# Kernel tuning notes

Measured on AMD Instinct MI355X. Metric: run time of the kernel, lower is better.

The kernel has to match this reference:

```python
import jax, jax.numpy as jnp
import numpy as np
from jax import lax

NUM_CLASSES = 5  # config['training']['num_classes_per_task']
EMBED_DIM = 64


def _conv(x, w, b, pad):
    y = lax.conv_general_dilated(x, w, (1, 1), [(pad, pad), (pad, pad)],
                                 dimension_numbers=('NCHW', 'OIHW', 'NCHW'))
    return y + b[None, :, None, None]


def _maxpool2(x):
    n, c, h, w = x.shape
    return x.reshape(n, c, h // 2, 2, w // 2, 2).max(axis=(3, 5))


def _lenet(x, c1w, c1b, c2w, c2b, f1w, f1b, f2w, f2b, f3w, f3b):
    h = _maxpool2(jax.nn.relu(_conv(x, c1w, c1b, pad=2)))   # [N,6,14,14]
    h = _maxpool2(jax.nn.relu(_conv(h, c2w, c2b, pad=0)))   # [N,16,5,5]
    h = h.reshape(h.shape[0], -1)                            # [N,400]
    h = jax.nn.relu(h @ f1w.T + f1b)                         # [N,120]
    h = jax.nn.relu(h @ f2w.T + f2b)                         # [N,84]
    return h @ f3w.T + f3b                                   # [N,64]


def setup_inputs() -> dict:
    key = jax.random.key(0)
    ks = jax.random.split(key, 12)
    s = 0.1
    return {
        'x': jax.random.normal(ks[0], (20480, 1, 28, 28), dtype=jnp.float32),
        'c1w': jax.random.normal(ks[1], (6, 1, 5, 5), dtype=jnp.float32) * s,
        'c1b': jnp.zeros((6,), dtype=jnp.float32),
        'c2w': jax.random.normal(ks[2], (16, 6, 5, 5), dtype=jnp.float32) * s,
        'c2b': jnp.zeros((16,), dtype=jnp.float32),
        'f1w': jax.random.normal(ks[3], (120, 400), dtype=jnp.float32) * s,
        'f1b': jnp.zeros((120,), dtype=jnp.float32),
        'f2w': jax.random.normal(ks[4], (84, 120), dtype=jnp.float32) * s,
        'f2b': jnp.zeros((84,), dtype=jnp.float32),
        'f3w': jax.random.normal(ks[5], (EMBED_DIM, 84), dtype=jnp.float32) * s,
        'f3b': jnp.zeros((EMBED_DIM,), dtype=jnp.float32),
    }


def reference(x, c1w, c1b, c2w, c2b, f1w, f1b, f2w, f2b, f3w, f3b):
    emb = _lenet(x, c1w, c1b, c2w, c2b, f1w, f1b, f2w, f2b, f3w, f3b)  # [N,D]
    # Source builds a flat prototypes list of all N*D scalars / num_classes,
    # but only indices 0..D-1 are ever read -> first embedding row / num_classes.
    proto = emb[0] / NUM_CLASSES                     # [D]
    s = jax.nn.softmax(emb, axis=1)                  # softmax over dim 1
    # fun_L(x, p) = sqrt((x-p)^2) = |x-p|
    logits = jnp.abs(s - proto[None, :])             # [N,D]
    batch_size = x.shape[0] // NUM_CLASSES
    return logits.reshape(batch_size, NUM_CLASSES, -1)
```

## Files before the change

kernel.cpp:

```cpp
#include <hip/hip_runtime.h>


__device__ __forceinline__ int xcd_swizzle(int orig, int nwg) {
    int xcd = orig & 7, q = nwg >> 3, r = nwg & 7;
    int base = (xcd < r) ? xcd * (q + 1) : r * (q + 1) + (xcd - r) * q;
    return base + (orig >> 3);
}

__global__ __launch_bounds__(256) void transpose_x(
    const float* __restrict__ x, float* __restrict__ xt, int nc)
{
    __shared__ float t[64][65];
    const int tx = threadIdx.x & 63, ty = threadIdx.x >> 6;
    const int p0 = blockIdx.x * 64, n0 = blockIdx.y * 64;
    #pragma unroll
    for (int rr = 0; rr < 16; ++rr) {
        int nl = rr * 4 + ty;
        int pp = p0 + tx;
        int pr = pp >> 5, pc = pp & 31;
        float v = 0.f;
        if (pr >= 2 && pr < 30 && pc >= 2 && pc < 30)
            v = x[(size_t)(n0 + nl) * 784 + (pr - 2) * 28 + (pc - 2)];
        t[tx][nl] = v;
    }
    __syncthreads();
    #pragma unroll
    for (int rr = 0; rr < 16; ++rr) {
        int pl = rr * 4 + ty;
        xt[(size_t)(p0 + pl) * nc + n0 + tx] = t[pl][tx];
    }
}

__global__ __launch_bounds__(256, 2) void conv1_bt(
    const float* __restrict__ xt, const float* __restrict__ c1w,
    const float* __restrict__ c1b, float* __restrict__ p1t, int nc)
{
    const int newid = xcd_swizzle(blockIdx.x, gridDim.x);
    const int grp = newid / 196, pos = newid - grp * 196;
    const int py = pos / 14, px = pos - py * 14;
    const int img = grp * 512 + threadIdx.x * 2;
    const float* pb = xt + (size_t)((2 * py) * 32 + 2 * px) * nc + img;

    float2 acc[24];
    #pragma unroll
    for (int i = 0; i < 24; ++i) acc[i] = make_float2(0.f, 0.f);

    #pragma unroll
    for (int r = 0; r < 6; ++r) {
        float2 row[6];
        #pragma unroll
        for (int cc = 0; cc < 6; ++cc)
            row[cc] = *(const float2*)&pb[(size_t)(r * 32 + cc) * nc];
        #pragma unroll
        for (int ch = 0; ch < 6; ++ch) {
            const float* wp = c1w + ch * 25;
            if (r <= 4) {
                #pragma unroll
                for (int kx = 0; kx < 5; ++kx) {
                    float w = wp[r * 5 + kx];
                    acc[ch*4+0].x += row[kx].x   * w;
                    acc[ch*4+0].y += row[kx].y   * w;
                    acc[ch*4+1].x += row[kx+1].x * w;
                    acc[ch*4+1].y += row[kx+1].y * w;
                }
            }
            if (r >= 1) {
                #pragma unroll
                for (int kx = 0; kx < 5; ++kx) {
                    float w = wp[(r - 1) * 5 + kx];
                    acc[ch*4+2].x += row[kx].x   * w;
                    acc[ch*4+2].y += row[kx].y   * w;
                    acc[ch*4+3].x += row[kx+1].x * w;
                    acc[ch*4+3].y += row[kx+1].y * w;
                }
            }
        }
    }
    #pragma unroll
    for (int ch = 0; ch < 6; ++ch) {
        float b = c1b[ch];
        float mx = fmaxf(fmaxf(acc[ch*4+0].x, acc[ch*4+1].x),
                         fmaxf(acc[ch*4+2].x, acc[ch*4+3].x)) + b;
        float my = fmaxf(fmaxf(acc[ch*4+0].y, acc[ch*4+1].y),
                         fmaxf(acc[ch*4+2].y, acc[ch*4+3].y)) + b;
        float2 o2 = make_float2(fmaxf(mx, 0.f), fmaxf(my, 0.f));
        *(float2*)&p1t[(size_t)(ch * 196 + pos) * nc + img] = o2;
    }
}

__global__ __launch_bounds__(256, 2) void conv2_bt(
    const float* __restrict__ p1t, const float* __restrict__ c2w,
    const float* __restrict__ c2b, float* __restrict__ ht, int nc)
{
    const int newid = xcd_swizzle(blockIdx.x, gridDim.x);
    const int grp = newid / 25, pos = newid - grp * 25;
    const int qy = pos / 5, qx = pos - qy * 5;
    const int img = grp * 256 + threadIdx.x;
    const int y0 = 2 * qy, x0 = 2 * qx;

    float acc[64];
    #pragma unroll
    for (int i = 0; i < 64; ++i) acc[i] = 0.f;

    #pragma unroll 1
    for (int ci = 0; ci < 6; ++ci) {
        const float* pb = p1t + (size_t)(ci * 196 + y0 * 14 + x0) * nc + img;
        #pragma unroll
        for (int r = 0; r < 6; ++r) {
            float row[6];
            #pragma unroll
            for (int cc = 0; cc < 6; ++cc)
                row[cc] = pb[(size_t)(r * 14 + cc) * nc];
            #pragma unroll
            for (int oc = 0; oc < 16; ++oc) {
                const float* wp = c2w + (oc * 6 + ci) * 25;
                if (r <= 4) {
                    #pragma unroll
                    for (int kx = 0; kx < 5; ++kx) {
                        float w = wp[r * 5 + kx];
                        acc[oc*4+0] += row[kx]   * w;
                        acc[oc*4+1] += row[kx+1] * w;
                    }
                }
                if (r >= 1) {
                    #pragma unroll
                    for (int kx = 0; kx < 5; ++kx) {
                        float w = wp[(r - 1) * 5 + kx];
                        acc[oc*4+2] += row[kx]   * w;
                        acc[oc*4+3] += row[kx+1] * w;
                    }
                }
            }
        }
    }
    #pragma unroll
    for (int oc = 0; oc < 16; ++oc) {
        float b = c2b[oc];
        float m = fmaxf(fmaxf(acc[oc*4+0], acc[oc*4+1]),
                        fmaxf(acc[oc*4+2], acc[oc*4+3])) + b;
        ht[(size_t)(oc * 25 + pos) * nc + img] = fmaxf(m, 0.f);
    }
}

__global__ __launch_bounds__(256) void fc1_bt(
    const float* __restrict__ ht, const float* __restrict__ f1w,
    const float* __restrict__ f1b, float* __restrict__ a1t, int nc)
{
    const int newid = xcd_swizzle(blockIdx.x, gridDim.x);
    const int grp = newid / 15, og = newid - grp * 15;
    const int img = grp * 512 + threadIdx.x * 2;
    const float* wb = f1w + og * 8 * 400;

    float2 acc[8];
    #pragma unroll
    for (int j = 0; j < 8; ++j) acc[j] = make_float2(0.f, 0.f);

    #pragma unroll 4
    for (int k = 0; k < 400; ++k) {
        float2 hv = *(const float2*)&ht[(size_t)k * nc + img];
        #pragma unroll
        for (int j = 0; j < 8; ++j) {
            float w = wb[j * 400 + k];
            acc[j].x += hv.x * w;
            acc[j].y += hv.y * w;
        }
    }
    #pragma unroll
    for (int j = 0; j < 8; ++j) {
        int o = og * 8 + j;
        float b = f1b[o];
        float2 o2 = make_float2(fmaxf(acc[j].x + b, 0.f),
                                fmaxf(acc[j].y + b, 0.f));
        *(float2*)&a1t[(size_t)o * nc + img] = o2;
    }
}

__global__ __launch_bounds__(256) void fc2_bt(
    const float* __restrict__ a1t, const float* __restrict__ f2w,
    const float* __restrict__ f2b, float* __restrict__ a2t, int nc)
{
    const int newid = xcd_swizzle(blockIdx.x, gridDim.x);
    const int grp = newid / 12, og = newid - grp * 12;
    const int img = grp * 512 + threadIdx.x * 2;
    const float* wb = f2w + og * 7 * 120;

    float2 acc[7];
    #pragma unroll
    for (int j = 0; j < 7; ++j) acc[j] = make_float2(0.f, 0.f);

    #pragma unroll 4
    for (int k = 0; k < 120; ++k) {
        float2 hv = *(const float2*)&a1t[(size_t)k * nc + img];
        #pragma unroll
        for (int j = 0; j < 7; ++j) {
            float w = wb[j * 120 + k];
            acc[j].x += hv.x * w;
            acc[j].y += hv.y * w;
        }
    }
    #pragma unroll
    for (int j = 0; j < 7; ++j) {
        int o = og * 7 + j;
        float b = f2b[o];
        float2 o2 = make_float2(fmaxf(acc[j].x + b, 0.f),
                                fmaxf(acc[j].y + b, 0.f));
        *(float2*)&a2t[(size_t)o * nc + img] = o2;
    }
}

__global__ __launch_bounds__(256) void fc3_bt(
    const float* __restrict__ a2t, const float* __restrict__ f3w,
    const float* __restrict__ f3b, float* __restrict__ embt,
    int nc, int Ntot, int n0)
{
    const int newid = xcd_swizzle(blockIdx.x, gridDim.x);
    const int grp = newid / 8, og = newid - grp * 8;
    const int limg = grp * 512 + threadIdx.x * 2;
    const float* wb = f3w + og * 8 * 84;

    float2 acc[8];
    #pragma unroll
    for (int j = 0; j < 8; ++j) acc[j] = make_float2(0.f, 0.f);

    #pragma unroll 4
    for (int k = 0; k < 84; ++k) {
        float2 hv = *(const float2*)&a2t[(size_t)k * nc + limg];
        #pragma unroll
        for (int j = 0; j < 8; ++j) {
            float w = wb[j * 84 + k];
            acc[j].x += hv.x * w;
            acc[j].y += hv.y * w;
        }
    }
    #pragma unroll
    for (int j = 0; j < 8; ++j) {
        int o = og * 8 + j;
        float b = f3b[o];
        float2 o2 = make_float2(acc[j].x + b, acc[j].y + b);
        *(float2*)&embt[(size_t)o * Ntot + n0 + limg] = o2;
    }
}

__global__ __launch_bounds__(256) void proto_head_t(
    const float* __restrict__ embt, float* __restrict__ out, int N)
{
    const int img = blockIdx.x * 256 + threadIdx.x;
    float v[64];
    float m = -1e30f;
    #pragma unroll
    for (int o = 0; o < 64; ++o) {
        v[o] = embt[(size_t)o * N + img];
        m = fmaxf(m, v[o]);
    }
    float s = 0.f;
    #pragma unroll
    for (int o = 0; o < 64; ++o) {
        v[o] = __expf(v[o] - m);
        s += v[o];
    }
    float inv = __frcp_rn(s);
    #pragma unroll
    for (int o = 0; o < 64; o += 4) {
        float4 r;
        r.x = fabsf(v[o+0] * inv - embt[(size_t)(o+0) * N] * 0.2f);
        r.y = fabsf(v[o+1] * inv - embt[(size_t)(o+1) * N] * 0.2f);
        r.z = fabsf(v[o+2] * inv - embt[(size_t)(o+2) * N] * 0.2f);
        r.w = fabsf(v[o+3] * inv - embt[(size_t)(o+3) * N] * 0.2f);
        *(float4*)&out[(size_t)img * 64 + o] = r;
    }
}

extern "C" void kernel_launch(void* const* d_in, const int* in_sizes, int n_in,
                              void* d_out, int out_size, void* d_ws, size_t ws_size,
                              hipStream_t stream)
{
    const float* x   = (const float*)d_in[0];
    const float* c1w = (const float*)d_in[1];
    const float* c1b = (const float*)d_in[2];
    const float* c2w = (const float*)d_in[3];
    const float* c2b = (const float*)d_in[4];
    const float* f1w = (const float*)d_in[5];
    const float* f1b = (const float*)d_in[6];
    const float* f2w = (const float*)d_in[7];
    const float* f2b = (const float*)d_in[8];
    const float* f3w = (const float*)d_in[9];
    const float* f3b = (const float*)d_in[10];
    float* out = (float*)d_out;

    const int N = in_sizes[0] / 784;
    float* base = (float*)d_ws;

    int c = 40;
    const int cands[] = {1, 2, 4, 5, 8, 10, 20, 40};
    for (int k = 0; k < 8; ++k) {
        int cd = cands[k];
        if (N % cd) continue;
        int ncq = N / cd;
        if (ncq % 512) continue;
        size_t need = (size_t)8800 * ncq + (size_t)256 * N;
        if (need <= ws_size) { c = cd; break; }
    }
    const int nc = N / c;

    float* xt   = base;
    float* p1t  = base + (size_t)1024 * nc;
    float* ht_  = base;
    float* a1t  = p1t;
    float* a2t  = p1t + (size_t)120 * nc;
    float* embt = base + (size_t)2200 * nc;

    for (int k = 0; k < c; ++k) {
        int n0 = k * nc;
        transpose_x<<<dim3(16, nc / 64), 256, 0, stream>>>(
            x + (size_t)n0 * 784, xt, nc);
        conv1_bt<<<196 * (nc / 512), 256, 0, stream>>>(
            xt, c1w, c1b, p1t, nc);
        conv2_bt<<<25 * (nc / 256), 256, 0, stream>>>(
            p1t, c2w, c2b, ht_, nc);
        fc1_bt<<<15 * (nc / 512), 256, 0, stream>>>(
            ht_, f1w, f1b, a1t, nc);
        fc2_bt<<<12 * (nc / 512), 256, 0, stream>>>(
            a1t, f2w, f2b, a2t, nc);
        fc3_bt<<<8 * (nc / 512), 256, 0, stream>>>(
            a2t, f3w, f3b, embt, nc, N, n0);
    }
    proto_head_t<<<N / 256, 256, 0, stream>>>(embt, out, N);
}
```

Baseline: 296.0 us.

## Split conv1 and conv2 output channels across blocks, process two images per thread

conv1 now splits its 6 output channels into two passes of 3 handled by separate blocks, halving the accumulator registers per thread. conv2 splits its 16 output channels into four groups of 4 and switches to float2 loads so each thread handles two images. The aim is lower register pressure, more blocks in flight, and wider memory accesses in conv2. The cost is that input rows are reloaded once per channel group (2x for conv1, 4x for conv2), which adds global or cache traffic.

```diff
diff --git a/kernel.cpp b/kernel.cpp
--- a/kernel.cpp
+++ b/kernel.cpp
@@ -36,14 +36,15 @@
     const float* __restrict__ c1b, float* __restrict__ p1t, int nc)
 {
     const int newid = xcd_swizzle(blockIdx.x, gridDim.x);
-    const int grp = newid / 196, pos = newid - grp * 196;
+    const int grp = newid / 392, rem = newid - grp * 392;
+    const int pass = rem / 196, pos = rem - pass * 196;
     const int py = pos / 14, px = pos - py * 14;
     const int img = grp * 512 + threadIdx.x * 2;
     const float* pb = xt + (size_t)((2 * py) * 32 + 2 * px) * nc + img;
 
-    float2 acc[24];
-    #pragma unroll
-    for (int i = 0; i < 24; ++i) acc[i] = make_float2(0.f, 0.f);
+    float2 acc[12];
+    #pragma unroll
+    for (int i = 0; i < 12; ++i) acc[i] = make_float2(0.f, 0.f);
 
     #pragma unroll
     for (int r = 0; r < 6; ++r) {
@@ -52,37 +53,38 @@
         for (int cc = 0; cc < 6; ++cc)
             row[cc] = *(const float2*)&pb[(size_t)(r * 32 + cc) * nc];
         #pragma unroll
-        for (int ch = 0; ch < 6; ++ch) {
-            const float* wp = c1w + ch * 25;
+        for (int c3 = 0; c3 < 3; ++c3) {
+            const float* wp = c1w + (pass * 3 + c3) * 25;
             if (r <= 4) {
                 #pragma unroll
                 for (int kx = 0; kx < 5; ++kx) {
                     float w = wp[r * 5 + kx];
-                    acc[ch*4+0].x += row[kx].x   * w;
-                    acc[ch*4+0].y += row[kx].y   * w;
-                    acc[ch*4+1].x += row[kx+1].x * w;
-                    acc[ch*4+1].y += row[kx+1].y * w;
+                    acc[c3*4+0].x += row[kx].x   * w;
+                    acc[c3*4+0].y += row[kx].y   * w;
+                    acc[c3*4+1].x += row[kx+1].x * w;
+                    acc[c3*4+1].y += row[kx+1].y * w;
                 }
             }
             if (r >= 1) {
                 #pragma unroll
                 for (int kx = 0; kx < 5; ++kx) {
                     float w = wp[(r - 1) * 5 + kx];
-                    acc[ch*4+2].x += row[kx].x   * w;
-                    acc[ch*4+2].y += row[kx].y   * w;
-                    acc[ch*4+3].x += row[kx+1].x * w;
-                    acc[ch*4+3].y += row[kx+1].y * w;
+                    acc[c3*4+2].x += row[kx].x   * w;
+                    acc[c3*4+2].y += row[kx].y   * w;
+                    acc[c3*4+3].x += row[kx+1].x * w;
+                    acc[c3*4+3].y += row[kx+1].y * w;
                 }
             }
         }
     }
     #pragma unroll
-    for (int ch = 0; ch < 6; ++ch) {
+    for (int c3 = 0; c3 < 3; ++c3) {
+        int ch = pass * 3 + c3;
         float b = c1b[ch];
-        float mx = fmaxf(fmaxf(acc[ch*4+0].x, acc[ch*4+1].x),
-                         fmaxf(acc[ch*4+2].x, acc[ch*4+3].x)) + b;
-        float my = fmaxf(fmaxf(acc[ch*4+0].y, acc[ch*4+1].y),
-                         fmaxf(acc[ch*4+2].y, acc[ch*4+3].y)) + b;
+        float mx = fmaxf(fmaxf(acc[c3*4+0].x, acc[c3*4+1].x),
+                         fmaxf(acc[c3*4+2].x, acc[c3*4+3].x)) + b;
+        float my = fmaxf(fmaxf(acc[c3*4+0].y, acc[c3*4+1].y),
+                         fmaxf(acc[c3*4+2].y, acc[c3*4+3].y)) + b;
         float2 o2 = make_float2(fmaxf(mx, 0.f), fmaxf(my, 0.f));
         *(float2*)&p1t[(size_t)(ch * 196 + pos) * nc + img] = o2;
     }
@@ -93,52 +95,61 @@
     const float* __restrict__ c2b, float* __restrict__ ht, int nc)
 {
     const int newid = xcd_swizzle(blockIdx.x, gridDim.x);
-    const int grp = newid / 25, pos = newid - grp * 25;
+    const int grp = newid / 100, rem = newid - grp * 100;
+    const int pass = rem / 25, pos = rem - pass * 25;
     const int qy = pos / 5, qx = pos - qy * 5;
-    const int img = grp * 256 + threadIdx.x;
+    const int img = grp * 512 + threadIdx.x * 2;
     const int y0 = 2 * qy, x0 = 2 * qx;
 
-    float acc[64];
-    #pragma unroll
-    for (int i = 0; i < 64; ++i) acc[i] = 0.f;
+    float2 acc[16];
+    #pragma unroll
+    for (int i = 0; i < 16; ++i) acc[i] = make_float2(0.f, 0.f);
 
     #pragma unroll 1
     for (int ci = 0; ci < 6; ++ci) {
         const float* pb = p1t + (size_t)(ci * 196 + y0 * 14 + x0) * nc + img;
         #pragma unroll
         for (int r = 0; r < 6; ++r) {
-            float row[6];
+            float2 row[6];
             #pragma unroll
             for (int cc = 0; cc < 6; ++cc)
-                row[cc] = pb[(size_t)(r * 14 + cc) * nc];
+                row[cc] = *(const float2*)&pb[(size_t)(r * 14 + cc) * nc];
             #pragma unroll
-            for (int oc = 0; oc < 16; ++oc) {
-                const float* wp = c2w + (oc * 6 + ci) * 25;
+            for (int o4 = 0; o4 < 4; ++o4) {
+                const float* wp = c2w + ((pass * 4 + o4) * 6 + ci) * 25;
                 if (r <= 4) {
                     #pragma unroll
                     for (int kx = 0; kx < 5; ++kx) {
                         float w = wp[r * 5 + kx];
-                        acc[oc*4+0] += row[kx]   * w;
-                        acc[oc*4+1] += row[kx+1] * w;
+                        acc[o4*4+0].x += row[kx].x   * w;
+                        acc[o4*4+0].y += row[kx].y   * w;
+                        acc[o4*4+1].x += row[kx+1].x * w;
+                        acc[o4*4+1].y += row[kx+1].y * w;
                     }
                 }
                 if (r >= 1) {
                     #pragma unroll
                     for (int kx = 0; kx < 5; ++kx) {
                         float w = wp[(r - 1) * 5 + kx];
-                        acc[oc*4+2] += row[kx]   * w;
-                        acc[oc*4+3] += row[kx+1] * w;
+                        acc[o4*4+2].x += row[kx].x   * w;
+                        acc[o4*4+2].y += row[kx].y   * w;
+                        acc[o4*4+3].x += row[kx+1].x * w;
+                        acc[o4*4+3].y += row[kx+1].y * w;
                     }
                 }
             }
         }
     }
     #pragma unroll
-    for (int oc = 0; oc < 16; ++oc) {
+    for (int o4 = 0; o4 < 4; ++o4) {
+        int oc = pass * 4 + o4;
         float b = c2b[oc];
-        float m = fmaxf(fmaxf(acc[oc*4+0], acc[oc*4+1]),
-                        fmaxf(acc[oc*4+2], acc[oc*4+3])) + b;
-        ht[(size_t)(oc * 25 + pos) * nc + img] = fmaxf(m, 0.f);
+        float mx = fmaxf(fmaxf(acc[o4*4+0].x, acc[o4*4+1].x),
+                         fmaxf(acc[o4*4+2].x, acc[o4*4+3].x)) + b;
+        float my = fmaxf(fmaxf(acc[o4*4+0].y, acc[o4*4+1].y),
+                         fmaxf(acc[o4*4+2].y, acc[o4*4+3].y)) + b;
+        float2 o2 = make_float2(fmaxf(mx, 0.f), fmaxf(my, 0.f));
+        *(float2*)&ht[(size_t)(oc * 25 + pos) * nc + img] = o2;
     }
 }
 
@@ -313,9 +324,9 @@
         int n0 = k * nc;
         transpose_x<<<dim3(16, nc / 64), 256, 0, stream>>>(
             x + (size_t)n0 * 784, xt, nc);
-        conv1_bt<<<196 * (nc / 512), 256, 0, stream>>>(
+        conv1_bt<<<392 * (nc / 512), 256, 0, stream>>>(
             xt, c1w, c1b, p1t, nc);
-        conv2_bt<<<25 * (nc / 256), 256, 0, stream>>>(
+        conv2_bt<<<100 * (nc / 512), 256, 0, stream>>>(
             p1t, c2w, c2b, ht_, nc);
         fc1_bt<<<15 * (nc / 512), 256, 0, stream>>>(
             ht_, f1w, f1b, a1t, nc);
```

Result: no change. 299.4 us (+1.1%).
